# Kernel tuning notes

Measured on AMD Instinct MI355X. Metric: run time of the kernel, lower is better.

The kernel has to match this reference:

```python
import jax, jax.numpy as jnp
import numpy as np

K = 2          # number of strips per spatial axis
ALPHA = 0.5    # boost strength
BETA = 0.5     # suppression floor
EPS = 1e-5     # BatchNorm eps


def _strip_attn(fm, w, b, gamma, beta, mean, var, axis):
    """1x1 conv (C->1) + BN(eval) + ReLU, per-strip avgpool along `axis`,
    softmax over the K strips, broadcast back to full resolution.
    fm: [B, C, W, H]; returns attention of shape [B, W] (axis=2) or [B, H] (axis=3)."""
    B, C, W, H = fm.shape
    conv = jnp.einsum('bcwh,c->bwh', fm, w) + b[0]          # [B, W, H]
    bn = (conv - mean[0]) * (gamma[0] / jnp.sqrt(var[0] + EPS)) + beta[0]
    act = jax.nn.relu(bn)
    if axis == 2:
        # strips along W: [B, K, W//K, H] -> mean over strip
        pooled = act.reshape(B, K, W // K, H).mean(axis=(2, 3))   # [B, K]
        rep = W // K
    else:
        # strips along H: [B, W, K, H//K] -> mean over strip
        pooled = act.reshape(B, W, K, H // K).mean(axis=(1, 3))   # [B, K]
        rep = W // K  # original code uses w // k for both repeats (w == h here)
    attn = jax.nn.softmax(pooled, axis=1)                     # [B, K]
    return jnp.repeat(attn, rep, axis=1)                      # [B, W] or [B, H]


def reference(fm, w_w, b_w, gamma_w, beta_w, mean_w, var_w,
              w_h, b_h, gamma_h, beta_h, mean_h, var_h):
    aw = _strip_attn(fm, w_w, b_w, gamma_w, beta_w, mean_w, var_w, axis=2)  # [B, W]
    ah = _strip_attn(fm, w_h, b_h, gamma_h, beta_h, mean_h, var_h, axis=3)  # [B, H]
    # fm_final: [B, 1, W, H] (broadcast over channels)
    fm_final = aw[:, None, :, None] * ah[:, None, None, :]
    fms_boost = fm + ALPHA * (fm * fm_final)
    # per-sample max over fm_final; suppress mask = 1.0 where below 0.95*max, else BETA
    fms_max = fm_final.max(axis=(1, 2, 3), keepdims=True)                   # [B,1,1,1]
    mask = jnp.where(fm_final < fms_max * 0.95, jnp.float32(1.0), jnp.float32(BETA))
    fms_suppress = fm * mask
    return fms_boost, fms_suppress


def setup_inputs() -> dict:
    key = jax.random.key(0)
    k1, k2, k3 = jax.random.split(key, 3)
    B, C, W, H = 32, 1024, 32, 32
    fan_out = 1  # kaiming fan_out for 1x1 conv with 1 output channel -> std = sqrt(2/1)
    std = float(np.sqrt(2.0 / 1.0))
    return {
        'fm': jax.random.normal(k1, (B, C, W, H), dtype=jnp.float32),
        'w_w': jax.random.normal(k2, (C,), dtype=jnp.float32) * std,
        'b_w': jnp.zeros((1,), jnp.float32),
        'gamma_w': jnp.ones((1,), jnp.float32),
        'beta_w': jnp.zeros((1,), jnp.float32),
        'mean_w': jnp.zeros((1,), jnp.float32),
        'var_w': jnp.ones((1,), jnp.float32),
        'w_h': jax.random.normal(k3, (C,), dtype=jnp.float32) * std,
        'b_h': jnp.zeros((1,), jnp.float32),
        'gamma_h': jnp.ones((1,), jnp.float32),
        'beta_h': jnp.zeros((1,), jnp.float32),
        'mean_h': jnp.zeros((1,), jnp.float32),
        'var_h': jnp.ones((1,), jnp.float32),
    }
```

## Files before the change

kernel.cpp:

```cpp
#include <hip/hip_runtime.h>

#define BN_EPS 1e-5f
#define ALPHA 0.5f
#define BETA 0.5f


__global__ __launch_bounds__(256) void k_conv(
    const float* __restrict__ fm, const float* __restrict__ wW,
    const float* __restrict__ wH, float* __restrict__ conv_w,
    float* __restrict__ conv_h) {
  const int blk = blockIdx.x;
  const int b = blk >> 4;
  const int cs = blk & 15;
  const int t = threadIdx.x;
  const int c0 = cs * 64;
  const float4* f4 = reinterpret_cast<const float4*>(fm) +
                     ((size_t)b * 1024 + c0) * 256 + t;
  float4 aw = {0.f, 0.f, 0.f, 0.f};
  float4 ah = {0.f, 0.f, 0.f, 0.f};
#pragma unroll 4
  for (int cc = 0; cc < 64; ++cc) {
    const float4 v = f4[(size_t)cc * 256];
    const float sw = wW[c0 + cc];
    const float sh = wH[c0 + cc];
    aw.x = fmaf(v.x, sw, aw.x);
    aw.y = fmaf(v.y, sw, aw.y);
    aw.z = fmaf(v.z, sw, aw.z);
    aw.w = fmaf(v.w, sw, aw.w);
    ah.x = fmaf(v.x, sh, ah.x);
    ah.y = fmaf(v.y, sh, ah.y);
    ah.z = fmaf(v.z, sh, ah.z);
    ah.w = fmaf(v.w, sh, ah.w);
  }
  float* cw = conv_w + b * 1024 + t * 4;
  float* ch = conv_h + b * 1024 + t * 4;
  atomicAdd(cw + 0, aw.x);
  atomicAdd(cw + 1, aw.y);
  atomicAdd(cw + 2, aw.z);
  atomicAdd(cw + 3, aw.w);
  atomicAdd(ch + 0, ah.x);
  atomicAdd(ch + 1, ah.y);
  atomicAdd(ch + 2, ah.z);
  atomicAdd(ch + 3, ah.w);
}

__global__ __launch_bounds__(64) void k_factors(
    const float* __restrict__ conv_w, const float* __restrict__ conv_h,
    const float* __restrict__ bw, const float* __restrict__ gw,
    const float* __restrict__ betw, const float* __restrict__ mw,
    const float* __restrict__ vw, const float* __restrict__ bh,
    const float* __restrict__ gh, const float* __restrict__ beth,
    const float* __restrict__ mh, const float* __restrict__ vh,
    float2* __restrict__ fac) {
  const int b = blockIdx.x;
  const int t = threadIdx.x;

  const float scale_w = gw[0] * rsqrtf(vw[0] + BN_EPS);
  const float shift_w = (bw[0] - mw[0]) * scale_w + betw[0];
  const float scale_h = gh[0] * rsqrtf(vh[0] + BN_EPS);
  const float shift_h = (bh[0] - mh[0]) * scale_h + beth[0];

  float s_w0 = 0.f, s_w1 = 0.f, s_h0 = 0.f, s_h1 = 0.f;
#pragma unroll
  for (int j = 0; j < 16; ++j) {
    const int e = t * 16 + j;
    const int w = e >> 5;
    const int h = e & 31;
    const float aw = fmaxf(fmaf(conv_w[b * 1024 + e], scale_w, shift_w), 0.f);
    const float ah = fmaxf(fmaf(conv_h[b * 1024 + e], scale_h, shift_h), 0.f);
    if (w < 16) s_w0 += aw; else s_w1 += aw;
    if (h < 16) s_h0 += ah; else s_h1 += ah;
  }
#pragma unroll
  for (int off = 32; off >= 1; off >>= 1) {
    s_w0 += __shfl_down(s_w0, off);
    s_w1 += __shfl_down(s_w1, off);
    s_h0 += __shfl_down(s_h0, off);
    s_h1 += __shfl_down(s_h1, off);
  }
  if (t == 0) {
    const float pw0 = s_w0 * (1.f / 512.f), pw1 = s_w1 * (1.f / 512.f);
    const float ph0 = s_h0 * (1.f / 512.f), ph1 = s_h1 * (1.f / 512.f);
    const float mwv = fmaxf(pw0, pw1);
    const float ew0 = __expf(pw0 - mwv), ew1 = __expf(pw1 - mwv);
    const float sw0 = ew0 / (ew0 + ew1), sw1 = ew1 / (ew0 + ew1);
    const float mhv = fmaxf(ph0, ph1);
    const float eh0 = __expf(ph0 - mhv), eh1 = __expf(ph1 - mhv);
    const float sh0 = eh0 / (eh0 + eh1), sh1 = eh1 / (eh0 + eh1);

    float f[4];
    f[0] = sw0 * sh0;
    f[1] = sw0 * sh1;
    f[2] = sw1 * sh0;
    f[3] = sw1 * sh1;
    const float fmax4 =
        fmaxf(fmaxf(f[0], f[1]), fmaxf(f[2], f[3]));
    const float thr = fmax4 * 0.95f;
#pragma unroll
    for (int q = 0; q < 4; ++q) {
      const float boost = 1.f + ALPHA * f[q];
      const float mask = (f[q] < thr) ? 1.f : BETA;
      fac[b * 4 + q] = make_float2(boost, mask);
    }
  }
}

__global__ __launch_bounds__(256) void k_out(
    const float* __restrict__ fm, const float2* __restrict__ fac,
    float* __restrict__ out0, float* __restrict__ out1) {
  const size_t i = (size_t)blockIdx.x * 256 + threadIdx.x;
  const size_t e = i * 4;
  const int b = (int)(e >> 20);
  const int w = (int)(e >> 5) & 31;
  const int h = (int)e & 31;
  const float2 f = fac[(b << 2) | ((w >> 4) << 1) | (h >> 4)];
  const float4 v = reinterpret_cast<const float4*>(fm)[i];
  float4 o0, o1;
  o0.x = v.x * f.x; o0.y = v.y * f.x; o0.z = v.z * f.x; o0.w = v.w * f.x;
  o1.x = v.x * f.y; o1.y = v.y * f.y; o1.z = v.z * f.y; o1.w = v.w * f.y;
  reinterpret_cast<float4*>(out0)[i] = o0;
  reinterpret_cast<float4*>(out1)[i] = o1;
}

extern "C" void kernel_launch(void* const* d_in, const int* in_sizes, int n_in,
                              void* d_out, int out_size, void* d_ws,
                              size_t ws_size, hipStream_t stream) {
  const float* fm = (const float*)d_in[0];
  const float* w_w = (const float*)d_in[1];
  const float* b_w = (const float*)d_in[2];
  const float* g_w = (const float*)d_in[3];
  const float* be_w = (const float*)d_in[4];
  const float* m_w = (const float*)d_in[5];
  const float* v_w = (const float*)d_in[6];
  const float* w_h = (const float*)d_in[7];
  const float* b_h = (const float*)d_in[8];
  const float* g_h = (const float*)d_in[9];
  const float* be_h = (const float*)d_in[10];
  const float* m_h = (const float*)d_in[11];
  const float* v_h = (const float*)d_in[12];

  float* ws = (float*)d_ws;
  float* conv_w = ws;
  float* conv_h = ws + 32768;
  float2* fac = (float2*)(ws + 65536);

  float* out0 = (float*)d_out;
  float* out1 = out0 + (size_t)32 * 1024 * 1024;

  hipMemsetAsync(d_ws, 0, 65536 * sizeof(float), stream);

  k_conv<<<32 * 16, 256, 0, stream>>>(fm, w_w, w_h, conv_w, conv_h);
  k_factors<<<32, 64, 0, stream>>>(conv_w, conv_h, b_w, g_w, be_w, m_w, v_w,
                                   b_h, g_h, be_h, m_h, v_h, fac);
  k_out<<<32768, 256, 0, stream>>>(fm, fac, out0, out1);
}
```

Baseline: 103.3 us.

## Fuse BN/ReLU/strip pooling into conv kernel and use nontemporal output stores

The conv kernel now assigns one block per (batch, row). Each block reduces all 1024 channels in shared memory, applies BN+ReLU, and atomically accumulates only the per-strip pooled sums, so the full conv maps are no longer written and re-read. The factors kernel shrinks to a single block, and the memset covers only 128 floats. The output kernel processes four float4 per thread with nontemporal stores to reduce cache pollution on the 256MB write stream. Risks are the extra shared-memory reduction cost and different launch shapes.

```diff
diff --git a/kernel.cpp b/kernel.cpp
--- a/kernel.cpp
+++ b/kernel.cpp
@@ -5,24 +5,47 @@
 #define BETA 0.5f
 
 
+typedef float vfloat4 __attribute__((ext_vector_type(4)));
+
 __global__ __launch_bounds__(256) void k_conv(
     const float* __restrict__ fm, const float* __restrict__ wW,
-    const float* __restrict__ wH, float* __restrict__ conv_w,
-    float* __restrict__ conv_h) {
-  const int blk = blockIdx.x;
-  const int b = blk >> 4;
-  const int cs = blk & 15;
+    const float* __restrict__ wH, const float* __restrict__ bw,
+    const float* __restrict__ gw, const float* __restrict__ betw,
+    const float* __restrict__ mw, const float* __restrict__ vw,
+    const float* __restrict__ bh, const float* __restrict__ gh,
+    const float* __restrict__ beth, const float* __restrict__ mh,
+    const float* __restrict__ vh, float* __restrict__ pooled_w,
+    float* __restrict__ pooled_h) {
+  __shared__ float lw[1024];
+  __shared__ float lh[1024];
+  __shared__ float4 part_w[32][8];
+  __shared__ float4 part_h[32][8];
+
   const int t = threadIdx.x;
-  const int c0 = cs * 64;
+  const int b = blockIdx.x >> 5;
+  const int row = blockIdx.x & 31;
+
+  {
+    const float4 a = reinterpret_cast<const float4*>(wW)[t];
+    const float4 c = reinterpret_cast<const float4*>(wH)[t];
+    reinterpret_cast<float4*>(lw)[t] = a;
+    reinterpret_cast<float4*>(lh)[t] = c;
+  }
+  __syncthreads();
+
+  const int c_off = t >> 3;
+  const int s4 = t & 7;
   const float4* f4 = reinterpret_cast<const float4*>(fm) +
-                     ((size_t)b * 1024 + c0) * 256 + t;
+                     ((size_t)(b * 1024 + c_off) * 256 + row * 8 + s4);
+
   float4 aw = {0.f, 0.f, 0.f, 0.f};
   float4 ah = {0.f, 0.f, 0.f, 0.f};
-#pragma unroll 4
-  for (int cc = 0; cc < 64; ++cc) {
-    const float4 v = f4[(size_t)cc * 256];
-    const float sw = wW[c0 + cc];
-    const float sh = wH[c0 + cc];
+#pragma unroll 8
+  for (int it = 0; it < 32; ++it) {
+    const int c = it * 32 + c_off;
+    const float4 v = f4[(size_t)it * 32 * 256];
+    const float sw = lw[c];
+    const float sh = lh[c];
     aw.x = fmaf(v.x, sw, aw.x);
     aw.y = fmaf(v.y, sw, aw.y);
     aw.z = fmaf(v.z, sw, aw.z);
@@ -32,94 +55,101 @@
     ah.z = fmaf(v.z, sh, ah.z);
     ah.w = fmaf(v.w, sh, ah.w);
   }
-  float* cw = conv_w + b * 1024 + t * 4;
-  float* ch = conv_h + b * 1024 + t * 4;
-  atomicAdd(cw + 0, aw.x);
-  atomicAdd(cw + 1, aw.y);
-  atomicAdd(cw + 2, aw.z);
-  atomicAdd(cw + 3, aw.w);
-  atomicAdd(ch + 0, ah.x);
-  atomicAdd(ch + 1, ah.y);
-  atomicAdd(ch + 2, ah.z);
-  atomicAdd(ch + 3, ah.w);
+  part_w[c_off][s4] = aw;
+  part_h[c_off][s4] = ah;
+  __syncthreads();
+
+  if (t < 8) {
+    const float scale_w = gw[0] * rsqrtf(vw[0] + BN_EPS);
+    const float shift_w = (bw[0] - mw[0]) * scale_w + betw[0];
+    const float scale_h = gh[0] * rsqrtf(vh[0] + BN_EPS);
+    const float shift_h = (bh[0] - mh[0]) * scale_h + beth[0];
+
+    float4 cw = {0.f, 0.f, 0.f, 0.f};
+    float4 ch = {0.f, 0.f, 0.f, 0.f};
+#pragma unroll
+    for (int g = 0; g < 32; ++g) {
+      const float4 pw = part_w[g][t];
+      const float4 ph = part_h[g][t];
+      cw.x += pw.x; cw.y += pw.y; cw.z += pw.z; cw.w += pw.w;
+      ch.x += ph.x; ch.y += ph.y; ch.z += ph.z; ch.w += ph.w;
+    }
+    float aws = fmaxf(fmaf(cw.x, scale_w, shift_w), 0.f) +
+                fmaxf(fmaf(cw.y, scale_w, shift_w), 0.f) +
+                fmaxf(fmaf(cw.z, scale_w, shift_w), 0.f) +
+                fmaxf(fmaf(cw.w, scale_w, shift_w), 0.f);
+    float ahs = fmaxf(fmaf(ch.x, scale_h, shift_h), 0.f) +
+                fmaxf(fmaf(ch.y, scale_h, shift_h), 0.f) +
+                fmaxf(fmaf(ch.z, scale_h, shift_h), 0.f) +
+                fmaxf(fmaf(ch.w, scale_h, shift_h), 0.f);
+    const int kh = (t >> 2) & 1;
+    float v0 = kh == 0 ? ahs : 0.f;
+    float v1 = kh == 1 ? ahs : 0.f;
+#pragma unroll
+    for (int off = 4; off >= 1; off >>= 1) {
+      aws += __shfl_xor(aws, off);
+      v0 += __shfl_xor(v0, off);
+      v1 += __shfl_xor(v1, off);
+    }
+    if (t == 0) {
+      const int kw = row >> 4;
+      atomicAdd(&pooled_w[b * 2 + kw], aws);
+      atomicAdd(&pooled_h[b * 2 + 0], v0);
+      atomicAdd(&pooled_h[b * 2 + 1], v1);
+    }
+  }
 }
 
 __global__ __launch_bounds__(64) void k_factors(
-    const float* __restrict__ conv_w, const float* __restrict__ conv_h,
-    const float* __restrict__ bw, const float* __restrict__ gw,
-    const float* __restrict__ betw, const float* __restrict__ mw,
-    const float* __restrict__ vw, const float* __restrict__ bh,
-    const float* __restrict__ gh, const float* __restrict__ beth,
-    const float* __restrict__ mh, const float* __restrict__ vh,
+    const float* __restrict__ pooled_w, const float* __restrict__ pooled_h,
     float2* __restrict__ fac) {
-  const int b = blockIdx.x;
-  const int t = threadIdx.x;
+  const int b = threadIdx.x;
+  if (b >= 32) return;
+  const float pw0 = pooled_w[b * 2 + 0] * (1.f / 512.f);
+  const float pw1 = pooled_w[b * 2 + 1] * (1.f / 512.f);
+  const float ph0 = pooled_h[b * 2 + 0] * (1.f / 512.f);
+  const float ph1 = pooled_h[b * 2 + 1] * (1.f / 512.f);
 
-  const float scale_w = gw[0] * rsqrtf(vw[0] + BN_EPS);
-  const float shift_w = (bw[0] - mw[0]) * scale_w + betw[0];
-  const float scale_h = gh[0] * rsqrtf(vh[0] + BN_EPS);
-  const float shift_h = (bh[0] - mh[0]) * scale_h + beth[0];
+  const float mwv = fmaxf(pw0, pw1);
+  const float ew0 = __expf(pw0 - mwv), ew1 = __expf(pw1 - mwv);
+  const float sw0 = ew0 / (ew0 + ew1), sw1 = ew1 / (ew0 + ew1);
+  const float mhv = fmaxf(ph0, ph1);
+  const float eh0 = __expf(ph0 - mhv), eh1 = __expf(ph1 - mhv);
+  const float sh0 = eh0 / (eh0 + eh1), sh1 = eh1 / (eh0 + eh1);
 
-  float s_w0 = 0.f, s_w1 = 0.f, s_h0 = 0.f, s_h1 = 0.f;
+  float f[4];
+  f[0] = sw0 * sh0;
+  f[1] = sw0 * sh1;
+  f[2] = sw1 * sh0;
+  f[3] = sw1 * sh1;
+  const float thr = fmaxf(fmaxf(f[0], f[1]), fmaxf(f[2], f[3])) * 0.95f;
 #pragma unroll
-  for (int j = 0; j < 16; ++j) {
-    const int e = t * 16 + j;
-    const int w = e >> 5;
-    const int h = e & 31;
-    const float aw = fmaxf(fmaf(conv_w[b * 1024 + e], scale_w, shift_w), 0.f);
-    const float ah = fmaxf(fmaf(conv_h[b * 1024 + e], scale_h, shift_h), 0.f);
-    if (w < 16) s_w0 += aw; else s_w1 += aw;
-    if (h < 16) s_h0 += ah; else s_h1 += ah;
-  }
-#pragma unroll
-  for (int off = 32; off >= 1; off >>= 1) {
-    s_w0 += __shfl_down(s_w0, off);
-    s_w1 += __shfl_down(s_w1, off);
-    s_h0 += __shfl_down(s_h0, off);
-    s_h1 += __shfl_down(s_h1, off);
-  }
-  if (t == 0) {
-    const float pw0 = s_w0 * (1.f / 512.f), pw1 = s_w1 * (1.f / 512.f);
-    const float ph0 = s_h0 * (1.f / 512.f), ph1 = s_h1 * (1.f / 512.f);
-    const float mwv = fmaxf(pw0, pw1);
-    const float ew0 = __expf(pw0 - mwv), ew1 = __expf(pw1 - mwv);
-    const float sw0 = ew0 / (ew0 + ew1), sw1 = ew1 / (ew0 + ew1);
-    const float mhv = fmaxf(ph0, ph1);
-    const float eh0 = __expf(ph0 - mhv), eh1 = __expf(ph1 - mhv);
-    const float sh0 = eh0 / (eh0 + eh1), sh1 = eh1 / (eh0 + eh1);
-
-    float f[4];
-    f[0] = sw0 * sh0;
-    f[1] = sw0 * sh1;
-    f[2] = sw1 * sh0;
-    f[3] = sw1 * sh1;
-    const float fmax4 =
-        fmaxf(fmaxf(f[0], f[1]), fmaxf(f[2], f[3]));
-    const float thr = fmax4 * 0.95f;
-#pragma unroll
-    for (int q = 0; q < 4; ++q) {
-      const float boost = 1.f + ALPHA * f[q];
-      const float mask = (f[q] < thr) ? 1.f : BETA;
-      fac[b * 4 + q] = make_float2(boost, mask);
-    }
+  for (int q = 0; q < 4; ++q) {
+    const float boost = 1.f + ALPHA * f[q];
+    const float mask = (f[q] < thr) ? 1.f : BETA;
+    fac[b * 4 + q] = make_float2(boost, mask);
   }
 }
 
 __global__ __launch_bounds__(256) void k_out(
     const float* __restrict__ fm, const float2* __restrict__ fac,
     float* __restrict__ out0, float* __restrict__ out1) {
-  const size_t i = (size_t)blockIdx.x * 256 + threadIdx.x;
-  const size_t e = i * 4;
-  const int b = (int)(e >> 20);
-  const int w = (int)(e >> 5) & 31;
-  const int h = (int)e & 31;
-  const float2 f = fac[(b << 2) | ((w >> 4) << 1) | (h >> 4)];
-  const float4 v = reinterpret_cast<const float4*>(fm)[i];
-  float4 o0, o1;
-  o0.x = v.x * f.x; o0.y = v.y * f.x; o0.z = v.z * f.x; o0.w = v.w * f.x;
-  o1.x = v.x * f.y; o1.y = v.y * f.y; o1.z = v.z * f.y; o1.w = v.w * f.y;
-  reinterpret_cast<float4*>(out0)[i] = o0;
-  reinterpret_cast<float4*>(out1)[i] = o1;
+  const size_t i0 = (size_t)blockIdx.x * 256 + threadIdx.x;
+  const vfloat4* fm4 = reinterpret_cast<const vfloat4*>(fm);
+  vfloat4* o0 = reinterpret_cast<vfloat4*>(out0);
+  vfloat4* o1 = reinterpret_cast<vfloat4*>(out1);
+#pragma unroll
+  for (int k = 0; k < 4; ++k) {
+    const size_t i = i0 + (size_t)k * 2097152;
+    const size_t e = i * 4;
+    const int b = (int)(e >> 20);
+    const int kw = ((int)(e >> 5) & 31) >> 4;
+    const int kh = ((int)e & 31) >> 4;
+    const float2 f = fac[(b << 2) | (kw << 1) | kh];
+    const vfloat4 v = fm4[i];
+    __builtin_nontemporal_store(v * f.x, &o0[i]);
+    __builtin_nontemporal_store(v * f.y, &o1[i]);
+  }
 }
 
 extern "C" void kernel_launch(void* const* d_in, const int* in_sizes, int n_in,
@@ -140,17 +170,18 @@
   const float* v_h = (const float*)d_in[12];
 
   float* ws = (float*)d_ws;
-  float* conv_w = ws;
-  float* conv_h = ws + 32768;
-  float2* fac = (float2*)(ws + 65536);
+  float* pooled_w = ws;
+  float* pooled_h = ws + 64;
+  float2* fac = (float2*)(ws + 128);
 
   float* out0 = (float*)d_out;
   float* out1 = out0 + (size_t)32 * 1024 * 1024;
 
-  hipMemsetAsync(d_ws, 0, 65536 * sizeof(float), stream);
+  hipMemsetAsync(d_ws, 0, 128 * sizeof(float), stream);
 
-  k_conv<<<32 * 16, 256, 0, stream>>>(fm, w_w, w_h, conv_w, conv_h);
-  k_factors<<<32, 64, 0, stream>>>(conv_w, conv_h, b_w, g_w, be_w, m_w, v_w,
-                                   b_h, g_h, be_h, m_h, v_h, fac);
-  k_out<<<32768, 256, 0, stream>>>(fm, fac, out0, out1);
+  k_conv<<<32 * 32, 256, 0, stream>>>(fm, w_w, w_h, b_w, g_w, be_w, m_w, v_w,
+                                      b_h, g_h, be_h, m_h, v_h, pooled_w,
+                                      pooled_h);
+  k_factors<<<1, 64, 0, stream>>>(pooled_w, pooled_h, fac);
+  k_out<<<8192, 256, 0, stream>>>(fm, fac, out0, out1);
 }
```

Result: no change. 102.5 us (-0.8%).
